# Kernel tuning notes

Measured on AMD Instinct MI355X. Metric: run time of the kernel, lower is better.

Reference implementation:

```python
import jax, jax.numpy as jnp
import numpy as np

B, S, K_IN = 8, 2048, 512
D_MODEL = 1024
N_INPUT = 2048
N_PROCESS = 4096
HIDDEN = 4096  # default hidden_dim = n_input * 2
K = 256


def setup_inputs() -> dict:
    key = jax.random.key(0)
    ks = jax.random.split(key, 7)
    return {
        "selected_activations": jax.random.normal(ks[0], (B, S, K_IN), dtype=jnp.float32),
        "selected_indices": jax.random.randint(ks[1], (B, K_IN), 0, N_INPUT),
        "k": K,
        "combination_weights": jax.random.normal(ks[2], (N_PROCESS, N_INPUT), dtype=jnp.float32) * np.float32(np.sqrt(2.0 / N_INPUT)),
        "output_projections": jax.random.normal(ks[3], (N_PROCESS, D_MODEL), dtype=jnp.float32) * np.float32(np.sqrt(2.0 / N_PROCESS)),
        "w1": jax.random.normal(ks[4], (HIDDEN, N_INPUT), dtype=jnp.float32) * np.float32(np.sqrt(2.0 / (N_INPUT + HIDDEN))),
        "b1": jnp.zeros((HIDDEN,), dtype=jnp.float32),
        "w2": jax.random.normal(ks[5], (N_PROCESS, HIDDEN), dtype=jnp.float32) * np.float32(np.sqrt(2.0 / (HIDDEN + N_PROCESS))),
        "b2": jnp.zeros((N_PROCESS,), dtype=jnp.float32),
    }


def reference(selected_activations, selected_indices, k, combination_weights,
              output_projections, w1, b1, w2, b2):
    bsz = selected_indices.shape[0]
    n_input = combination_weights.shape[1]

    # Per-batch gather of combination weights: [B, k_in, n_process]
    sel_w = combination_weights.T[selected_indices]

    # Process activations: [B, S, n_process], exact (erf) GELU like torch F.gelu
    process_activations = jax.nn.gelu(
        jnp.einsum('bsk,bkp->bsp', selected_activations, sel_w), approximate=False)

    # One-hot style input-selection mask via scatter: [B, n_input]
    input_selection = jnp.zeros((bsz, n_input), dtype=jnp.float32)
    input_selection = input_selection.at[jnp.arange(bsz)[:, None], selected_indices].set(1.0)

    # Combination analyzer MLP: Linear -> GELU -> Linear
    h = jax.nn.gelu(input_selection @ w1.T + b1, approximate=False)
    combination_relevance = h @ w2.T + b2  # [B, n_process]

    # Router scores and top-k process selection
    activation_scores = process_activations.max(axis=1)  # [B, n_process]
    final_scores = activation_scores * jax.nn.sigmoid(combination_relevance)
    _, process_indices = jax.lax.top_k(final_scores, k)  # [B, k]

    # Gather selected process activations [B, S, k] and projections [B, k, d_model]
    sel_pa = jnp.take_along_axis(process_activations, process_indices[:, None, :], axis=2)
    sel_proj = output_projections[process_indices]

    # Final projection: [B, S, d_model]
    return jnp.einsum('bsk,bkd->bsd', sel_pa, sel_proj)
```

## Files before the change

kernel.cpp:

```cpp
#include <hip/hip_runtime.h>
#include <math.h>

#define B 8
#define S 2048
#define KIN 512
#define NIN 2048
#define NP 4096
#define HID 4096
#define DM 1024
#define TOPK 256

typedef __bf16 bf16x8 __attribute__((ext_vector_type(8)));
typedef __bf16 bf16x4 __attribute__((ext_vector_type(4)));
typedef float f32x4 __attribute__((ext_vector_type(4)));

__device__ __forceinline__ float gelu_exact(float x) {
    return 0.5f * x * (1.0f + erff(x * 0.70710678118654752440f));
}

__device__ __forceinline__ void atomicMaxFloat(float* addr, float val) {
    if (val >= 0.0f) atomicMax((int*)addr, __float_as_int(val));
    else             atomicMin((unsigned int*)addr, __float_as_uint(val));
}

__device__ __forceinline__ void async_copy16(void* lds, const void* g) {
    __builtin_amdgcn_global_load_lds(
        (__attribute__((address_space(1))) void*)g,
        (__attribute__((address_space(3))) void*)lds, 16, 0, 0);
}

__global__ __launch_bounds__(256) void init_kernel(float* scores, float* relacc,
                                                   float* hacc, unsigned* maskb,
                                                   int* selcnt) {
    int t = blockIdx.x * blockDim.x + threadIdx.x;
    if (t < B * NP)  { scores[t] = __int_as_float(0xFF800000); relacc[t] = 0.f; }
    if (t < B * HID) hacc[t] = 0.f;
    if (t < NIN)     maskb[t] = 0u;
    if (t < B)       selcnt[t] = 0;
}

__global__ __launch_bounds__(256) void scatter_maskbits(const int* __restrict__ idx,
                                                        unsigned* __restrict__ maskb) {
    int t = blockIdx.x * blockDim.x + threadIdx.x;
    if (t >= B * KIN) return;
    int b = t / KIN;
    atomicOr(&maskb[idx[t]], 1u << b);
}

__global__ __launch_bounds__(256) void pack_A(const float* __restrict__ A,
                                              __bf16* __restrict__ Apack) {
    size_t t = (size_t)blockIdx.x * 256 + threadIdx.x;
    size_t f = t * 4;
    size_t rowi = f >> 9;
    int j = (int)(f & 511);
    float4 v = *(const float4*)(A + f);
    __bf16 h0 = (__bf16)v.x, h1 = (__bf16)v.y, h2 = (__bf16)v.z, h3 = (__bf16)v.w;
    bf16x4 hv = {h0, h1, h2, h3};
    bf16x4 lv = {(__bf16)(v.x - (float)h0), (__bf16)(v.y - (float)h1),
                 (__bf16)(v.z - (float)h2), (__bf16)(v.w - (float)h3)};
    __bf16* orow = Apack + rowi * 1024;
    *(bf16x4*)(orow + j) = hv;
    *(bf16x4*)(orow + 512 + j) = lv;
}

__global__ __launch_bounds__(256) void gather_pack_w(const float* __restrict__ cw,
                                                     const int* __restrict__ idx,
                                                     __bf16* __restrict__ wpack) {
    __shared__ float rowbuf[4][NIN];
    __shared__ int sidx[B][KIN];
    int p0 = blockIdx.x * 4;
    int tid = threadIdx.x;
    for (int t = tid; t < B * KIN; t += 256) sidx[t >> 9][t & 511] = idx[t];
#pragma unroll
    for (int r = 0; r < 4; ++r)
        for (int c = tid; c < NIN / 4; c += 256)
            *(float4*)&rowbuf[r][c * 4] = *(const float4*)&cw[(size_t)(p0 + r) * NIN + c * 4];
    __syncthreads();
#pragma unroll
    for (int r = 0; r < 4; ++r) {
        int p = p0 + r;
        for (int b = 0; b < B; ++b) {
            __bf16* orow = wpack + ((size_t)b * NP + p) * 1024;
            for (int j = tid; j < KIN; j += 256) {
                float x = rowbuf[r][sidx[b][j]];
                __bf16 hh = (__bf16)x;
                orow[j] = hh;
                orow[512 + j] = (__bf16)(x - (float)hh);
            }
        }
    }
}

template <int EPI, int NSEG, int KSEG, int LDA, int LDB, int BROWS, int LDOUT>
__global__ __launch_bounds__(256) void mfma_gemm(const __bf16* __restrict__ Ap,
                                                 const __bf16* __restrict__ Bp,
                                                 void* __restrict__ outp) {
    __shared__ __align__(16) __bf16 As[128 * 64];
    __shared__ __align__(16) __bf16 Ws[128 * 64];
    const int b = blockIdx.z;
    const int s0 = blockIdx.x * 128;
    const int p0 = blockIdx.y * 128;
    const int tid = threadIdx.x;
    const int w = tid >> 6, lane = tid & 63;
    const int wr = w >> 1, wc = w & 1;
    const int ldRow = lane >> 3;
    const int ldCol = ((lane & 7) ^ (ldRow & 7)) * 8;
    const int fr = lane & 15;
    const int fq = lane >> 4;
    const __bf16* Ab = Ap + ((size_t)b * S + s0) * LDA;
    const __bf16* Bb = Bp + ((size_t)b * BROWS + p0) * LDB;

    f32x4 acc[4][4] = {};

    for (int seg = 0; seg < NSEG; ++seg) {
        const int aoff = (seg == 1) ? KSEG : 0;
        const int boff = (seg == 2) ? KSEG : 0;
        for (int k0 = 0; k0 < KSEG; k0 += 64) {
            __syncthreads();
#pragma unroll
            for (int i = 0; i < 4; ++i) {
                const __bf16* g = Ab + (size_t)(w * 32 + i * 8 + ldRow) * LDA + aoff + k0 + ldCol;
                async_copy16(&As[(w * 32 + i * 8) * 64], g);
            }
#pragma unroll
            for (int i = 0; i < 4; ++i) {
                const __bf16* g = Bb + (size_t)(w * 32 + i * 8 + ldRow) * LDB + boff + k0 + ldCol;
                async_copy16(&Ws[(w * 32 + i * 8) * 64], g);
            }
            __syncthreads();
#pragma unroll
            for (int ks = 0; ks < 2; ++ks) {
                bf16x8 af[4], bfr[4];
#pragma unroll
                for (int i = 0; i < 4; ++i) {
                    int R = wr * 64 + i * 16 + fr;
                    af[i] = *(const bf16x8*)&As[R * 64 + (((ks * 4 + fq) ^ (R & 7)) * 8)];
                }
#pragma unroll
                for (int j = 0; j < 4; ++j) {
                    int R = wc * 64 + j * 16 + fr;
                    bfr[j] = *(const bf16x8*)&Ws[R * 64 + (((ks * 4 + fq) ^ (R & 7)) * 8)];
                }
#pragma unroll
                for (int i = 0; i < 4; ++i)
#pragma unroll
                    for (int j = 0; j < 4; ++j)
                        acc[i][j] = __builtin_amdgcn_mfma_f32_16x16x32_bf16(af[i], bfr[j], acc[i][j], 0, 0, 0);
            }
        }
    }

    if constexpr (EPI == 0) {
        float* scores = (float*)outp;
#pragma unroll
        for (int j = 0; j < 4; ++j) {
            float m = -INFINITY;
#pragma unroll
            for (int i = 0; i < 4; ++i)
#pragma unroll
                for (int r = 0; r < 4; ++r) m = fmaxf(m, gelu_exact(acc[i][j][r]));
            m = fmaxf(m, __shfl_xor(m, 16));
            m = fmaxf(m, __shfl_xor(m, 32));
            if (fq == 0)
                atomicMaxFloat(&scores[(size_t)b * LDOUT + p0 + wc * 64 + j * 16 + fr], m);
        }
    } else if constexpr (EPI == 1) {
        __bf16* o = (__bf16*)outp;
#pragma unroll
        for (int i = 0; i < 4; ++i)
#pragma unroll
            for (int r = 0; r < 4; ++r) {
                size_t row = (size_t)b * S + s0 + wr * 64 + i * 16 + fq * 4 + r;
#pragma unroll
                for (int j = 0; j < 4; ++j)
                    o[row * LDOUT + p0 + wc * 64 + j * 16 + fr] = (__bf16)gelu_exact(acc[i][j][r]);
            }
    } else {
        float* o = (float*)outp;
#pragma unroll
        for (int i = 0; i < 4; ++i)
#pragma unroll
            for (int r = 0; r < 4; ++r) {
                size_t row = (size_t)b * S + s0 + wr * 64 + i * 16 + fq * 4 + r;
#pragma unroll
                for (int j = 0; j < 4; ++j)
                    o[row * LDOUT + p0 + wc * 64 + j * 16 + fr] = acc[i][j][r];
            }
    }
}

__global__ __launch_bounds__(256) void mlp1_part(const float* __restrict__ w1,
                                                 const unsigned* __restrict__ maskb,
                                                 float* __restrict__ hacc) {
    __shared__ unsigned smb[512];
    int i0 = blockIdx.x * 64;
    int c0 = blockIdx.y * 512;
    int tid = threadIdx.x;
    for (int c = tid; c < 512; c += 256) smb[c] = maskb[c0 + c];
    __syncthreads();
    int r = tid >> 2, cq = tid & 3;
    const float* row = w1 + (size_t)(i0 + r) * NIN + c0;
    float acc[B] = {};
    for (int it = 0; it < 32; ++it) {
        int c = it * 16 + cq * 4;
        float4 v = *(const float4*)(row + c);
        float vv[4] = {v.x, v.y, v.z, v.w};
#pragma unroll
        for (int e = 0; e < 4; ++e) {
            unsigned mb = smb[c + e];
#pragma unroll
            for (int bb = 0; bb < B; ++bb)
                if (mb & (1u << bb)) acc[bb] += vv[e];
        }
    }
#pragma unroll
    for (int bb = 0; bb < B; ++bb)
        atomicAdd(&hacc[bb * HID + i0 + r], acc[bb]);
}

__global__ __launch_bounds__(256) void fin1(const float* __restrict__ hacc,
                                            const float* __restrict__ b1,
                                            float* __restrict__ h) {
    int t = blockIdx.x * 256 + threadIdx.x;
    if (t < B * HID) h[t] = gelu_exact(hacc[t] + b1[t & (HID - 1)]);
}

__global__ __launch_bounds__(256) void mlp2_part(const float* __restrict__ w2,
                                                 const float* __restrict__ h,
                                                 float* __restrict__ relacc) {
    __shared__ float sh[B][512];
    int p0 = blockIdx.x * 64;
    int c0 = blockIdx.y * 512;
    int tid = threadIdx.x;
    for (int i = tid; i < B * 128; i += 256) {
        int bb = i >> 7, c4 = i & 127;
        *(float4*)&sh[bb][c4 * 4] = *(const float4*)&h[(size_t)bb * HID + c0 + c4 * 4];
    }
    __syncthreads();
    int r = tid >> 2, cq = tid & 3;
    const float* row = w2 + (size_t)(p0 + r) * HID + c0;
    float acc[B] = {};
    for (int it = 0; it < 32; ++it) {
        int c = it * 16 + cq * 4;
        float4 v = *(const float4*)(row + c);
#pragma unroll
        for (int bb = 0; bb < B; ++bb)
            acc[bb] += v.x * sh[bb][c] + v.y * sh[bb][c + 1] + v.z * sh[bb][c + 2] + v.w * sh[bb][c + 3];
    }
#pragma unroll
    for (int bb = 0; bb < B; ++bb)
        atomicAdd(&relacc[bb * NP + p0 + r], acc[bb]);
}

__global__ __launch_bounds__(256) void fin2(const float* __restrict__ relacc,
                                            const float* __restrict__ b2,
                                            float* __restrict__ scores) {
    int t = blockIdx.x * 256 + threadIdx.x;
    if (t >= B * NP) return;
    float rel = relacc[t] + b2[t & (NP - 1)];
    scores[t] *= 1.0f / (1.0f + expf(-rel));
}

__global__ __launch_bounds__(256) void topk_select(const float* __restrict__ scores,
                                                   int* __restrict__ selidx,
                                                   int* __restrict__ selcnt) {
    __shared__ float sc[NP];
    int b = blockIdx.y;
    int p = blockIdx.x * 256 + threadIdx.x;
    for (int c = threadIdx.x; c < NP; c += 256) sc[c] = scores[(size_t)b * NP + c];
    __syncthreads();
    float my = sc[p];
    int cnt = 0;
    for (int q = 0; q < NP; ++q) {
        float v = sc[q];
        cnt += (v > my) || (v == my && q < p);
    }
    if (cnt < TOPK) {
        int pos = atomicAdd(&selcnt[b], 1);
        selidx[b * TOPK + pos] = p;
    }
}

__global__ __launch_bounds__(256) void wsel_gather(const __bf16* __restrict__ wpack,
                                                   const int* __restrict__ selidx,
                                                   __bf16* __restrict__ wsel) {
    int kk = blockIdx.x, b = blockIdx.y;
    int sel = selidx[b * TOPK + kk];
    const unsigned* src = (const unsigned*)(wpack + ((size_t)b * NP + sel) * 1024);
    unsigned* dst = (unsigned*)(wsel + ((size_t)b * TOPK + kk) * 512);
    dst[threadIdx.x] = src[threadIdx.x];
}

__global__ __launch_bounds__(256) void projT_gather(const float* __restrict__ proj,
                                                    const int* __restrict__ selidx,
                                                    __bf16* __restrict__ PT) {
    __shared__ float tile[64][68];
    __shared__ int sel[64];
    int b = blockIdx.z, d0 = blockIdx.x * 64, k0 = blockIdx.y * 64;
    int tid = threadIdx.x;
    if (tid < 64) sel[tid] = selidx[b * TOPK + k0 + tid];
    __syncthreads();
    for (int r = 0; r < 4; ++r) {
        int kk = r * 16 + (tid >> 4);
        float4 v = *(const float4*)&proj[(size_t)sel[kk] * DM + d0 + (tid & 15) * 4];
        *(float4*)&tile[kk][(tid & 15) * 4] = v;
    }
    __syncthreads();
    for (int r = 0; r < 16; ++r) {
        int dd = r * 4 + (tid >> 6);
        int kk = tid & 63;
        PT[((size_t)b * DM + d0 + dd) * TOPK + k0 + kk] = (__bf16)tile[kk][dd];
    }
}

extern "C" void kernel_launch(void* const* d_in, const int* in_sizes, int n_in,
                              void* d_out, int out_size, void* d_ws, size_t ws_size,
                              hipStream_t stream) {
    const float* A    = (const float*)d_in[0];
    const int*   idx  = (const int*)d_in[1];
    const float* cw   = (const float*)d_in[3];
    const float* proj = (const float*)d_in[4];
    const float* w1   = (const float*)d_in[5];
    const float* b1   = (const float*)d_in[6];
    const float* w2   = (const float*)d_in[7];
    const float* b2   = (const float*)d_in[8];
    float* out = (float*)d_out;

    char* ws = (char*)d_ws;
    size_t off = 0;
    auto alloc = [&](size_t bytes) {
        void* p = ws + off;
        off += (bytes + 255) & ~(size_t)255;
        return p;
    };
    __bf16* Apack = (__bf16*)alloc((size_t)B * S * 1024 * 2);
    __bf16* Wpack = (__bf16*)alloc((size_t)B * NP * 1024 * 2);
    __bf16* selpa = (__bf16*)alloc((size_t)B * S * TOPK * 2);
    __bf16* PT    = (__bf16*)alloc((size_t)B * DM * TOPK * 2);
    __bf16* Wsel  = (__bf16*)alloc((size_t)B * TOPK * 512 * 2);
    float* scores = (float*)alloc((size_t)B * NP * 4);
    float* relacc = (float*)alloc((size_t)B * NP * 4);
    float* hacc   = (float*)alloc((size_t)B * HID * 4);
    float* h      = (float*)alloc((size_t)B * HID * 4);
    unsigned* maskb = (unsigned*)alloc((size_t)NIN * 4);
    int* selidx   = (int*)alloc((size_t)B * TOPK * 4);
    int* selcnt   = (int*)alloc((size_t)B * 4);

    init_kernel<<<dim3((B * HID + 255) / 256), 256, 0, stream>>>(scores, relacc, hacc, maskb, selcnt);
    scatter_maskbits<<<dim3((B * KIN + 255) / 256), 256, 0, stream>>>(idx, maskb);
    pack_A<<<dim3((B * S * KIN / 4) / 256), 256, 0, stream>>>(A, Apack);
    gather_pack_w<<<dim3(NP / 4), 256, 0, stream>>>(cw, idx, Wpack);

    mfma_gemm<0, 3, 512, 1024, 1024, NP, NP>
        <<<dim3(S / 128, NP / 128, B), 256, 0, stream>>>(Apack, Wpack, (void*)scores);

    mlp1_part<<<dim3(HID / 64, NIN / 512), 256, 0, stream>>>(w1, maskb, hacc);
    fin1<<<dim3((B * HID + 255) / 256), 256, 0, stream>>>(hacc, b1, h);
    mlp2_part<<<dim3(NP / 64, HID / 512), 256, 0, stream>>>(w2, h, relacc);
    fin2<<<dim3((B * NP + 255) / 256), 256, 0, stream>>>(relacc, b2, scores);

    topk_select<<<dim3(NP / 256, B), 256, 0, stream>>>(scores, selidx, selcnt);

    wsel_gather<<<dim3(TOPK, B), 256, 0, stream>>>(Wpack, selidx, Wsel);
    projT_gather<<<dim3(DM / 64, TOPK / 64, B), 256, 0, stream>>>(proj, selidx, PT);

    mfma_gemm<1, 1, 512, 1024, 512, TOPK, TOPK>
        <<<dim3(S / 128, TOPK / 128, B), 256, 0, stream>>>(Apack, Wsel, (void*)selpa);

    mfma_gemm<2, 1, 256, 256, 256, DM, DM>
        <<<dim3(S / 128, DM / 128, B), 256, 0, stream>>>(selpa, PT, (void*)out);
}
```

Baseline: 746.3 us.

## Add 256x256 double-buffered MFMA GEMM for score pass with min/max GELU epilogue

Adds a new 512-thread GEMM kernel with 256x256 output tiles, double-buffered async LDS staging interleaved with MFMA phases, barriers and s_setprio. It is used for the large score GEMM, raising data reuse per loaded tile and overlapping global loads with compute. The score epilogue now reduces raw min and max per column and applies GELU only to those two values, instead of applying erf-GELU to every element. The cost is much larger LDS use and register pressure, which may limit occupancy.

Measured after the change: 682.6 us. 1.09x faster.

```diff
diff --git a/kernel.cpp b/kernel.cpp
--- a/kernel.cpp
+++ b/kernel.cpp
@@ -150,41 +150,218 @@
         }
     }
 
+    if constexpr (EPI == 1) {
+        __bf16* o = (__bf16*)outp;
+#pragma unroll
+        for (int i = 0; i < 4; ++i)
+#pragma unroll
+            for (int r = 0; r < 4; ++r) {
+                size_t row = (size_t)b * S + s0 + wr * 64 + i * 16 + fq * 4 + r;
+#pragma unroll
+                for (int j = 0; j < 4; ++j)
+                    o[row * LDOUT + p0 + wc * 64 + j * 16 + fr] = (__bf16)gelu_exact(acc[i][j][r]);
+            }
+    } else {
+        float* o = (float*)outp;
+#pragma unroll
+        for (int i = 0; i < 4; ++i)
+#pragma unroll
+            for (int r = 0; r < 4; ++r) {
+                size_t row = (size_t)b * S + s0 + wr * 64 + i * 16 + fq * 4 + r;
+#pragma unroll
+                for (int j = 0; j < 4; ++j)
+                    o[row * LDOUT + p0 + wc * 64 + j * 16 + fr] = acc[i][j][r];
+            }
+    }
+}
+
+__device__ __forceinline__ void stage64(__bf16* ldsTile, const __bf16* gRow0,
+                                        int rbase, int ldg, int koff, int w, int lane) {
+    const int rr = lane >> 3;
+    const int gc = ((lane & 7) ^ rr) * 8;
+    const __bf16* g = gRow0 + (size_t)(rbase + w * 8 + rr) * ldg + (koff + gc);
+    async_copy16(ldsTile + (rbase + w * 8) * 64, g);
+}
+
+__device__ __forceinline__ void read_frags4(const __bf16* base, int row0, int fr,
+                                            int fq, int kk, bf16x8* f) {
+#pragma unroll
+    for (int i = 0; i < 4; ++i) {
+        int R = row0 + i * 16 + fr;
+        f[i] = *(const bf16x8*)&base[R * 64 + (((kk * 4 + fq) ^ (R & 7)) * 8)];
+    }
+}
+
+template <int EPI, int NSEG, int KSEG, int LDA, int LDB, int BROWS, int LDOUT>
+__global__ __launch_bounds__(512, 2) void mfma_gemm256(const __bf16* __restrict__ Ap,
+                                                       const __bf16* __restrict__ Bp,
+                                                       void* __restrict__ outp) {
+    constexpr int TPS = KSEG / 64;
+    constexpr int NT = NSEG * TPS;
+    __shared__ __align__(16) __bf16 As[2][256 * 64];
+    __shared__ __align__(16) __bf16 Ws[2][256 * 64];
+    const int b = blockIdx.z;
+    const int s0 = blockIdx.x * 256;
+    const int p0 = blockIdx.y * 256;
+    const int tid = threadIdx.x;
+    const int w = tid >> 6, lane = tid & 63;
+    const int wr = w >> 2, wc = w & 3;
+    const int fr = lane & 15, fq = lane >> 4;
+    const __bf16* Ab = Ap + ((size_t)b * S + s0) * LDA;
+    const __bf16* Bb = Bp + ((size_t)b * BROWS + p0) * LDB;
+
+    auto offs = [&](int t, int& ao, int& bo) {
+        int seg = t / TPS, k0 = (t % TPS) * 64;
+        ao = ((NSEG == 3 && seg == 1) ? KSEG : 0) + k0;
+        bo = ((NSEG == 3 && seg == 2) ? KSEG : 0) + k0;
+    };
+
+    f32x4 acc[8][4] = {};
+
+    {
+        int ao, bo;
+        offs(0, ao, bo);
+        stage64(&As[0][0], Ab, 0, LDA, ao, w, lane);
+        stage64(&As[0][0], Ab, 128, LDA, ao, w, lane);
+        stage64(&As[0][0], Ab, 64, LDA, ao, w, lane);
+        stage64(&As[0][0], Ab, 192, LDA, ao, w, lane);
+        stage64(&Ws[0][0], Bb, 0, LDB, bo, w, lane);
+        stage64(&Ws[0][0], Bb, 128, LDB, bo, w, lane);
+        stage64(&Ws[0][0], Bb, 64, LDB, bo, w, lane);
+        stage64(&Ws[0][0], Bb, 192, LDB, bo, w, lane);
+        if (NT > 1) {
+            offs(1, ao, bo);
+            stage64(&As[1][0], Ab, 0, LDA, ao, w, lane);
+            stage64(&As[1][0], Ab, 128, LDA, ao, w, lane);
+            stage64(&Ws[1][0], Bb, 0, LDB, bo, w, lane);
+            stage64(&Ws[1][0], Bb, 128, LDB, bo, w, lane);
+            asm volatile("s_waitcnt vmcnt(4)");
+        } else {
+            asm volatile("s_waitcnt vmcnt(0)");
+        }
+        __builtin_amdgcn_s_barrier();
+    }
+
+    for (int t = 0; t < NT; ++t) {
+        __bf16* Asb = &As[t & 1][0];
+        __bf16* Wsb = &Ws[t & 1][0];
+        __bf16* Asn = &As[(t & 1) ^ 1][0];
+        __bf16* Wsn = &Ws[(t & 1) ^ 1][0];
+        bf16x8 af[4], bfr[4];
+
+        read_frags4(Asb, wr * 128, fr, fq, 0, af);
+        read_frags4(Wsb, wc * 64, fr, fq, 0, bfr);
+        if (t + 1 < NT) {
+            int ao, bo;
+            offs(t + 1, ao, bo);
+            stage64(Asn, Ab, 64, LDA, ao, w, lane);
+            stage64(Asn, Ab, 192, LDA, ao, w, lane);
+            stage64(Wsn, Bb, 64, LDB, bo, w, lane);
+            stage64(Wsn, Bb, 192, LDB, bo, w, lane);
+        }
+        __builtin_amdgcn_s_barrier();
+        asm volatile("s_waitcnt lgkmcnt(0)");
+        __builtin_amdgcn_s_setprio(1);
+#pragma unroll
+        for (int mi = 0; mi < 4; ++mi)
+#pragma unroll
+            for (int nj = 0; nj < 4; ++nj)
+                acc[mi][nj] = __builtin_amdgcn_mfma_f32_16x16x32_bf16(af[mi], bfr[nj], acc[mi][nj], 0, 0, 0);
+        __builtin_amdgcn_s_setprio(0);
+        __builtin_amdgcn_s_barrier();
+
+        read_frags4(Asb, wr * 128 + 64, fr, fq, 0, af);
+        __builtin_amdgcn_s_barrier();
+        asm volatile("s_waitcnt lgkmcnt(0)");
+        __builtin_amdgcn_s_setprio(1);
+#pragma unroll
+        for (int mi = 0; mi < 4; ++mi)
+#pragma unroll
+            for (int nj = 0; nj < 4; ++nj)
+                acc[4 + mi][nj] = __builtin_amdgcn_mfma_f32_16x16x32_bf16(af[mi], bfr[nj], acc[4 + mi][nj], 0, 0, 0);
+        __builtin_amdgcn_s_setprio(0);
+        __builtin_amdgcn_s_barrier();
+
+        read_frags4(Asb, wr * 128, fr, fq, 1, af);
+        read_frags4(Wsb, wc * 64, fr, fq, 1, bfr);
+        __builtin_amdgcn_s_barrier();
+        asm volatile("s_waitcnt lgkmcnt(0)");
+        __builtin_amdgcn_s_setprio(1);
+#pragma unroll
+        for (int mi = 0; mi < 4; ++mi)
+#pragma unroll
+            for (int nj = 0; nj < 4; ++nj)
+                acc[mi][nj] = __builtin_amdgcn_mfma_f32_16x16x32_bf16(af[mi], bfr[nj], acc[mi][nj], 0, 0, 0);
+        __builtin_amdgcn_s_setprio(0);
+        __builtin_amdgcn_s_barrier();
+
+        read_frags4(Asb, wr * 128 + 64, fr, fq, 1, af);
+        if (t + 2 < NT) {
+            int ao, bo;
+            offs(t + 2, ao, bo);
+            stage64(Asb, Ab, 0, LDA, ao, w, lane);
+            stage64(Asb, Ab, 128, LDA, ao, w, lane);
+            stage64(Wsb, Bb, 0, LDB, bo, w, lane);
+            stage64(Wsb, Bb, 128, LDB, bo, w, lane);
+            asm volatile("s_waitcnt vmcnt(4)");
+        } else {
+            asm volatile("s_waitcnt vmcnt(0)");
+        }
+        __builtin_amdgcn_s_barrier();
+        asm volatile("s_waitcnt lgkmcnt(0)");
+        __builtin_amdgcn_s_setprio(1);
+#pragma unroll
+        for (int mi = 0; mi < 4; ++mi)
+#pragma unroll
+            for (int nj = 0; nj < 4; ++nj)
+                acc[4 + mi][nj] = __builtin_amdgcn_mfma_f32_16x16x32_bf16(af[mi], bfr[nj], acc[4 + mi][nj], 0, 0, 0);
+        __builtin_amdgcn_s_setprio(0);
+        __builtin_amdgcn_s_barrier();
+    }
+
     if constexpr (EPI == 0) {
         float* scores = (float*)outp;
 #pragma unroll
-        for (int j = 0; j < 4; ++j) {
-            float m = -INFINITY;
-#pragma unroll
-            for (int i = 0; i < 4; ++i)
-#pragma unroll
-                for (int r = 0; r < 4; ++r) m = fmaxf(m, gelu_exact(acc[i][j][r]));
-            m = fmaxf(m, __shfl_xor(m, 16));
-            m = fmaxf(m, __shfl_xor(m, 32));
-            if (fq == 0)
-                atomicMaxFloat(&scores[(size_t)b * LDOUT + p0 + wc * 64 + j * 16 + fr], m);
+        for (int nj = 0; nj < 4; ++nj) {
+            float mx = -INFINITY, mn = INFINITY;
+#pragma unroll
+            for (int mi = 0; mi < 8; ++mi)
+#pragma unroll
+                for (int r = 0; r < 4; ++r) {
+                    float v = acc[mi][nj][r];
+                    mx = fmaxf(mx, v);
+                    mn = fminf(mn, v);
+                }
+            mx = fmaxf(mx, __shfl_xor(mx, 16));
+            mx = fmaxf(mx, __shfl_xor(mx, 32));
+            mn = fminf(mn, __shfl_xor(mn, 16));
+            mn = fminf(mn, __shfl_xor(mn, 32));
+            if (fq == 0) {
+                float m = fmaxf(gelu_exact(mx), gelu_exact(mn));
+                atomicMaxFloat(&scores[(size_t)b * LDOUT + p0 + wc * 64 + nj * 16 + fr], m);
+            }
         }
     } else if constexpr (EPI == 1) {
         __bf16* o = (__bf16*)outp;
 #pragma unroll
-        for (int i = 0; i < 4; ++i)
+        for (int mi = 0; mi < 8; ++mi)
 #pragma unroll
             for (int r = 0; r < 4; ++r) {
-                size_t row = (size_t)b * S + s0 + wr * 64 + i * 16 + fq * 4 + r;
-#pragma unroll
-                for (int j = 0; j < 4; ++j)
-                    o[row * LDOUT + p0 + wc * 64 + j * 16 + fr] = (__bf16)gelu_exact(acc[i][j][r]);
+                size_t row = (size_t)b * S + s0 + wr * 128 + mi * 16 + fq * 4 + r;
+#pragma unroll
+                for (int nj = 0; nj < 4; ++nj)
+                    o[row * LDOUT + p0 + wc * 64 + nj * 16 + fr] = (__bf16)gelu_exact(acc[mi][nj][r]);
             }
     } else {
         float* o = (float*)outp;
 #pragma unroll
-        for (int i = 0; i < 4; ++i)
+        for (int mi = 0; mi < 8; ++mi)
 #pragma unroll
             for (int r = 0; r < 4; ++r) {
-                size_t row = (size_t)b * S + s0 + wr * 64 + i * 16 + fq * 4 + r;
-#pragma unroll
-                for (int j = 0; j < 4; ++j)
-                    o[row * LDOUT + p0 + wc * 64 + j * 16 + fr] = acc[i][j][r];
+                size_t row = (size_t)b * S + s0 + wr * 128 + mi * 16 + fq * 4 + r;
+#pragma unroll
+                for (int nj = 0; nj < 4; ++nj)
+                    o[row * LDOUT + p0 + wc * 64 + nj * 16 + fr] = acc[mi][nj][r];
             }
     }
 }
@@ -351,8 +528,8 @@
     pack_A<<<dim3((B * S * KIN / 4) / 256), 256, 0, stream>>>(A, Apack);
     gather_pack_w<<<dim3(NP / 4), 256, 0, stream>>>(cw, idx, Wpack);
 
-    mfma_gemm<0, 3, 512, 1024, 1024, NP, NP>
-        <<<dim3(S / 128, NP / 128, B), 256, 0, stream>>>(Apack, Wpack, (void*)scores);
+    mfma_gemm256<0, 3, 512, 1024, 1024, NP, NP>
+        <<<dim3(S / 256, NP / 256, B), 512, 0, stream>>>(Apack, Wpack, (void*)scores);
 
     mlp1_part<<<dim3(HID / 64, NIN / 512), 256, 0, stream>>>(w1, maskb, hacc);
     fin1<<<dim3((B * HID + 255) / 256), 256, 0, stream>>>(hacc, b1, h);
```
